# Optimization experiments

Hardware: AMD Instinct MI355X
Metric: run time of the kernel (lower is better)

The kernel has to match this reference:

```python
import jax, jax.numpy as jnp
import numpy as np

# ViT-Small config
L, D, H, HD = 12, 384, 6, 64
P, IMG, NCLS = 16, 224, 1000
NPATCH = (IMG // P) ** 2  # 196
GAMMA, MIN_TOKENS, EPS = 0.5, 16, 1e-6
SCALE = HD ** -0.5


def _ln(x, w, b, eps=1e-6):
    mu = jnp.mean(x, axis=-1, keepdims=True)
    var = jnp.var(x, axis=-1, keepdims=True)
    return (x - mu) * jax.lax.rsqrt(var + eps) * w + b


def _qkv_split(xn, w, b):
    # xn: [B, Nt, D] -> q,k,v each [B, H, Nt, HD]
    B, Nt, _ = xn.shape
    qkv = (xn @ w.T + b).reshape(B, Nt, 3, H, HD).transpose(2, 0, 3, 1, 4)
    return qkv[0], qkv[1], qkv[2]


def _vit_forward(x, patch_w, patch_b, cls_token, pos_embed,
                 ln1_w, ln1_b, qkv_w, qkv_b, proj_w, proj_b,
                 ln2_w, ln2_b, fc1_w, fc1_b, fc2_w, fc2_b,
                 norm_w, norm_b, head_w, head_b, keep_schedule=None):
    B = x.shape[0]
    # patch embed: conv stride 16 -> [B, D, 14, 14] -> [B, 196, D]
    xp = jax.lax.conv_general_dilated(x, patch_w, (P, P), 'VALID',
                                      dimension_numbers=('NCHW', 'OIHW', 'NCHW'))
    xp = xp.reshape(B, D, NPATCH).transpose(0, 2, 1) + patch_b
    cls = jnp.broadcast_to(cls_token, (B, 1, D))
    xt = jnp.concatenate([cls, xp], axis=1) + pos_embed  # [B, 197, D]

    N = NPATCH
    prev_mass = jnp.asarray(1.0, jnp.float32)
    schedule = []
    for l in range(L):
        if keep_schedule is not None:
            keep_idx = keep_schedule[l]
        elif N > MIN_TOKENS:
            # CLS-only attention importance scoring (cheap pass)
            xn = _ln(xt, ln1_w[l], ln1_b[l])
            q, k, v = _qkv_split(xn, qkv_w[l], qkv_b[l])
            a_cls = jax.nn.softmax(jnp.einsum('bhqd,bhkd->bhqk', q[:, :, :1], k) * SCALE, axis=-1)[:, :, 0, :]  # [B,H,Nt]
            vnorm = jnp.linalg.norm(v, axis=-1)  # [B,H,Nt]
            imp = (a_cls * vnorm).mean(axis=1)   # [B,Nt]
            imp_p = imp[:, 1:]                   # patch importance
            mass = jnp.mean(imp_p.sum(-1) / (imp.sum(-1) + EPS))
            keep_ratio = float(jnp.clip(GAMMA * mass / (prev_mass + EPS), 0.0, 1.0))
            N_next = max(MIN_TOKENS, int(N * keep_ratio))
            if N_next < N:
                scores = imp_p.mean(0)  # shared keep set across batch (index_select semantics)
                top = jax.lax.top_k(scores, N_next)[1]
                keep_idx = jnp.concatenate([jnp.zeros((1,), jnp.int32),
                                            jnp.sort(top).astype(jnp.int32) + 1])
            else:
                keep_idx = None
            prev_mass = mass
        else:
            keep_idx = None
        schedule.append(keep_idx)
        if keep_idx is not None:
            xt = jnp.take(xt, keep_idx, axis=1)
            N = int(keep_idx.shape[0]) - 1

        # full transformer block on surviving tokens
        Nt = xt.shape[1]
        xn = _ln(xt, ln1_w[l], ln1_b[l])
        q, k, v = _qkv_split(xn, qkv_w[l], qkv_b[l])
        a = jax.nn.softmax(jnp.einsum('bhqd,bhkd->bhqk', q, k) * SCALE, axis=-1)
        o = jnp.einsum('bhqk,bhkd->bhqd', a, v).transpose(0, 2, 1, 3).reshape(B, Nt, D)
        xt = xt + o @ proj_w[l].T + proj_b[l]
        h = _ln(xt, ln2_w[l], ln2_b[l])
        h = jax.nn.gelu(h @ fc1_w[l].T + fc1_b[l], approximate=False)
        xt = xt + h @ fc2_w[l].T + fc2_b[l]

    xt = _ln(xt, norm_w, norm_b)
    logits = xt[:, 0] @ head_w.T + head_b
    return logits, schedule


def setup_inputs() -> dict:
    key = jax.random.key(0)
    ks = jax.random.split(key, 10)
    rn = lambda k, s, sc=0.02: jax.random.normal(k, s, jnp.float32) * sc
    return {
        'x': jax.random.normal(ks[0], (64, 3, IMG, IMG), jnp.float32),
        'patch_w': rn(ks[1], (D, 3, P, P)),
        'patch_b': jnp.zeros((D,), jnp.float32),
        'cls_token': rn(ks[2], (1, 1, D)),
        'pos_embed': rn(ks[3], (1, NPATCH + 1, D)),
        'ln1_w': jnp.ones((L, D), jnp.float32), 'ln1_b': jnp.zeros((L, D), jnp.float32),
        'qkv_w': rn(ks[4], (L, 3 * D, D)), 'qkv_b': jnp.zeros((L, 3 * D), jnp.float32),
        'proj_w': rn(ks[5], (L, D, D)), 'proj_b': jnp.zeros((L, D), jnp.float32),
        'ln2_w': jnp.ones((L, D), jnp.float32), 'ln2_b': jnp.zeros((L, D), jnp.float32),
        'fc1_w': rn(ks[6], (L, 4 * D, D)), 'fc1_b': jnp.zeros((L, 4 * D), jnp.float32),
        'fc2_w': rn(ks[7], (L, D, 4 * D)), 'fc2_b': jnp.zeros((L, D), jnp.float32),
        'norm_w': jnp.ones((D,), jnp.float32), 'norm_b': jnp.zeros((D,), jnp.float32),
        'head_w': rn(ks[8], (NCLS, D)), 'head_b': jnp.zeros((NCLS,), jnp.float32),
    }


def reference(x, patch_w, patch_b, cls_token, pos_embed, ln1_w, ln1_b, qkv_w, qkv_b,
              proj_w, proj_b, ln2_w, ln2_b, fc1_w, fc1_b, fc2_w, fc2_b,
              norm_w, norm_b, head_w, head_b):
    logits, _ = _vit_forward(x, patch_w, patch_b, cls_token, pos_embed, ln1_w, ln1_b,
                             qkv_w, qkv_b, proj_w, proj_b, ln2_w, ln2_b,
                             fc1_w, fc1_b, fc2_w, fc2_b, norm_w, norm_b, head_w, head_b)
    return logits
```

## Files before the change

### kernel.cpp

```cpp
#include <hip/hip_runtime.h>
#include <hip/hip_bf16.h>

static constexpr int kL = 12;
static constexpr int kD = 384;
static constexpr int kH = 6;
static constexpr int kB = 64;
static constexpr int kNP = 196;
static constexpr int kBAND = 197;
static constexpr int kNCLS = 1000;
static constexpr float kSCALE = 0.125f;
static constexpr float kEPS = 1e-6f;
static constexpr size_t kWQ = (size_t)kB * kH * kBAND * 64;

typedef __attribute__((ext_vector_type(8))) short short8;
typedef __attribute__((ext_vector_type(4))) float f32x4;

__device__ __forceinline__ float gelu_f(float x) {
    return 0.5f * x * (1.0f + erff(x * 0.70710678118654752440f));
}
__device__ __forceinline__ unsigned short f2bf(float x) {
    __hip_bfloat16 h = __float2bfloat16(x);
    return *(unsigned short*)&h;
}

__global__ __launch_bounds__(384) void k_init(int* si, float* sf,
                                              const float* __restrict__ cls,
                                              const float* __restrict__ pos,
                                              float* __restrict__ xtA,
                                              float2* __restrict__ pstats) {
    int b = blockIdx.x, c = threadIdx.x;
    float v = cls[c] + pos[c];
    xtA[(size_t)b * kBAND * kD + c] = v;
    __shared__ float r1[384], r2[384];
    r1[c] = v; r2[c] = v * v;
    __syncthreads();
    if (c < 128) { r1[c] += r1[c + 128] + r1[c + 256]; r2[c] += r2[c + 128] + r2[c + 256]; }
    __syncthreads();
    for (int st = 64; st; st >>= 1) {
        if (c < st) { r1[c] += r1[c + st]; r2[c] += r2[c + st]; }
        __syncthreads();
    }
    if (c == 0) {
        pstats[(size_t)(b * kBAND) * 8 + 0] = make_float2(r1[0], r2[0]);
#pragma unroll
        for (int nn = 1; nn < 6; ++nn) pstats[(size_t)(b * kBAND) * 8 + nn] = make_float2(0.f, 0.f);
        if (b == 0) { si[0] = kBAND; sf[0] = 1.0f; }
    }
}

__global__ __launch_bounds__(256) void k_cvtall(
    const float* __restrict__ s0, const float* __restrict__ s1, const float* __restrict__ s2,
    const float* __restrict__ s3, const float* __restrict__ s4,
    __hip_bfloat16* __restrict__ d0, __hip_bfloat16* __restrict__ d1, __hip_bfloat16* __restrict__ d2,
    __hip_bfloat16* __restrict__ d3, __hip_bfloat16* __restrict__ d4) {
    const int c0 = 73728, c1 = 1400832, c2 = 1843200, c3 = 3612672, c4 = 5382144;
    int stride = gridDim.x * 256;
    for (int i = blockIdx.x * 256 + threadIdx.x; i < c4; i += stride) {
        const float* src; __hip_bfloat16* dst; int off;
        if (i < c0)      { src = s0; dst = d0; off = i; }
        else if (i < c1) { src = s1; dst = d1; off = i - c0; }
        else if (i < c2) { src = s2; dst = d2; off = i - c1; }
        else if (i < c3) { src = s3; dst = d3; off = i - c2; }
        else             { src = s4; dst = d4; off = i - c3; }
        float4 v = ((const float4*)src)[off];
        dst[4 * off + 0] = __float2bfloat16(v.x);
        dst[4 * off + 1] = __float2bfloat16(v.y);
        dst[4 * off + 2] = __float2bfloat16(v.z);
        dst[4 * off + 3] = __float2bfloat16(v.w);
    }
}

__global__ __launch_bounds__(256) void k_im2col(const float* __restrict__ x, __hip_bfloat16* __restrict__ A) {
    int pt = blockIdx.x;
    int b = pt / kNP, t = pt - b * kNP;
    int py = t / 14, px = t - py * 14;
    const float* xb = x + (size_t)b * 3 * 224 * 224;
    __hip_bfloat16* arow = A + (size_t)pt * 768;
    for (int k = threadIdx.x; k < 768; k += 256) {
        int c = k >> 8;
        int r = k & 255;
        int ky = r >> 4, kx = r & 15;
        arow[k] = __float2bfloat16(xb[((size_t)c * 224 + py * 16 + ky) * 224 + px * 16 + kx]);
    }
}

template<int OUT_BF16, int ACT_GELU, int MODE, int LNA, int STATS>
__global__ __launch_bounds__(256) void k_mgemm(
    const void* __restrict__ Av, int lda,
    const unsigned short* __restrict__ W, int K,
    const float* __restrict__ bias,
    void* __restrict__ Cv, int ldc,
    const float* __restrict__ R,
    const int* __restrict__ keepR,
    const float* __restrict__ lnw, const float* __restrict__ lnb,
    int rT, int nT, int band,
    const int* __restrict__ NtPtr, int ntConst,
    const float2* __restrict__ pstatsIn, float2* __restrict__ pstatsOut)
{
    __shared__ __align__(16) unsigned char pool[18432];
    unsigned short (*As)[72] = (unsigned short (*)[72])pool;
    unsigned short (*Ws)[72] = (unsigned short (*)[72])(pool + 9216);
    float (*Cs)[66] = (float (*)[66])pool;
    unsigned short (*Cu)[76] = (unsigned short (*)[76])pool;
    __shared__ float mus[64], rss[64];

    int Nt = NtPtr ? NtPtr[0] : ntConst;
    unsigned int rowsTotal = (unsigned int)kB * (unsigned int)Nt;

    int L = blockIdx.x;
    int xcd = L & 7;
    int m = L >> 3;
    int n = m % nT;
    int r = (m / nT) * 8 + xcd;
    if (r >= rT) return;
    unsigned int r0 = (unsigned int)r * 64;
    int n0 = n * 64;
    if (r0 >= rowsTotal) return;

    int tid = threadIdx.x;
    int srow = tid >> 3;
    int scol = (tid & 7) << 3;

    unsigned int rv0 = r0 + srow, rv1 = r0 + srow + 32;
    bool v0 = rv0 < rowsTotal, v1 = rv1 < rowsTotal;
    const unsigned short* ah0 = nullptr; const unsigned short* ah1 = nullptr;
    const float* af0 = nullptr; const float* af1 = nullptr;
    if (v0) {
        unsigned int bb = rv0 / (unsigned int)Nt, tt = rv0 - bb * Nt;
        size_t prow = (size_t)bb * band + tt;
        if (LNA) af0 = (const float*)Av + prow * lda;
        else     ah0 = (const unsigned short*)Av + prow * lda;
    }
    if (v1) {
        unsigned int bb = rv1 / (unsigned int)Nt, tt = rv1 - bb * Nt;
        size_t prow = (size_t)bb * band + tt;
        if (LNA) af1 = (const float*)Av + prow * lda;
        else     ah1 = (const unsigned short*)Av + prow * lda;
    }
    const unsigned short* wp0 = W + (size_t)(n0 + srow) * K;
    const unsigned short* wp1 = W + (size_t)(n0 + srow + 32) * K;

    float mu0 = 0.f, rs0 = 0.f, mu1 = 0.f, rs1 = 0.f;
    if (LNA) {
        if (tid < 64) {
            unsigned int rv = r0 + tid;
            float mu = 0.f, rsd = 0.f;
            if (rv < rowsTotal) {
                unsigned int bb = rv / (unsigned int)Nt, tt = rv - bb * Nt;
                const float2* ps = pstatsIn + ((size_t)bb * band + tt) * 8;
                float s1 = 0.f, s2 = 0.f;
#pragma unroll
                for (int nn = 0; nn < 6; ++nn) { float2 p = ps[nn]; s1 += p.x; s2 += p.y; }
                mu = s1 * (1.f / 384.f);
                float var = fmaxf(s2 * (1.f / 384.f) - mu * mu, 0.f);
                rsd = rsqrtf(var + kEPS);
            }
            mus[tid] = mu; rss[tid] = rsd;
        }
        __syncthreads();
        mu0 = mus[srow]; rs0 = rss[srow];
        mu1 = mus[srow + 32]; rs1 = rss[srow + 32];
    }

    int wave = tid >> 6, lane = tid & 63;
    int wr32 = ((wave >> 1) & 1) * 32, wc32 = (wave & 1) * 32;
    int l15 = lane & 15, l4 = lane >> 4;

    f32x4 acc00 = {}, acc01 = {}, acc10 = {}, acc11 = {};

    for (int k0 = 0; k0 < K; k0 += 64) {
        uint4 zero = make_uint4(0, 0, 0, 0);
        uint4 a0 = zero, a1 = zero;
        uint4 w0 = *(const uint4*)(wp0 + k0 + scol);
        uint4 w1 = *(const uint4*)(wp1 + k0 + scol);
        if (LNA) {
            float4 lw0 = *(const float4*)(lnw + k0 + scol);
            float4 lw1 = *(const float4*)(lnw + k0 + scol + 4);
            float4 lb0 = *(const float4*)(lnb + k0 + scol);
            float4 lb1 = *(const float4*)(lnb + k0 + scol + 4);
            if (v0) {
                float4 x0 = *(const float4*)(af0 + k0 + scol);
                float4 x1 = *(const float4*)(af0 + k0 + scol + 4);
                unsigned short p[8];
                p[0] = f2bf((x0.x - mu0) * rs0 * lw0.x + lb0.x);
                p[1] = f2bf((x0.y - mu0) * rs0 * lw0.y + lb0.y);
                p[2] = f2bf((x0.z - mu0) * rs0 * lw0.z + lb0.z);
                p[3] = f2bf((x0.w - mu0) * rs0 * lw0.w + lb0.w);
                p[4] = f2bf((x1.x - mu0) * rs0 * lw1.x + lb1.x);
                p[5] = f2bf((x1.y - mu0) * rs0 * lw1.y + lb1.y);
                p[6] = f2bf((x1.z - mu0) * rs0 * lw1.z + lb1.z);
                p[7] = f2bf((x1.w - mu0) * rs0 * lw1.w + lb1.w);
                a0 = *(uint4*)p;
            }
            if (v1) {
                float4 x0 = *(const float4*)(af1 + k0 + scol);
                float4 x1 = *(const float4*)(af1 + k0 + scol + 4);
                unsigned short p[8];
                p[0] = f2bf((x0.x - mu1) * rs1 * lw0.x + lb0.x);
                p[1] = f2bf((x0.y - mu1) * rs1 * lw0.y + lb0.y);
                p[2] = f2bf((x0.z - mu1) * rs1 * lw0.z + lb0.z);
                p[3] = f2bf((x0.w - mu1) * rs1 * lw0.w + lb0.w);
                p[4] = f2bf((x1.x - mu1) * rs1 * lw1.x + lb1.x);
                p[5] = f2bf((x1.y - mu1) * rs1 * lw1.y + lb1.y);
                p[6] = f2bf((x1.z - mu1) * rs1 * lw1.z + lb1.z);
                p[7] = f2bf((x1.w - mu1) * rs1 * lw1.w + lb1.w);
                a1 = *(uint4*)p;
            }
        } else {
            a0 = v0 ? *(const uint4*)(ah0 + k0 + scol) : zero;
            a1 = v1 ? *(const uint4*)(ah1 + k0 + scol) : zero;
        }
        __syncthreads();
        *(uint4*)&As[srow][scol] = a0;
        *(uint4*)&As[srow + 32][scol] = a1;
        *(uint4*)&Ws[srow][scol] = w0;
        *(uint4*)&Ws[srow + 32][scol] = w1;
        __syncthreads();
#pragma unroll
        for (int ks = 0; ks < 2; ++ks) {
            short8 af_0 = *(const short8*)&As[wr32 + l15][ks * 32 + l4 * 8];
            short8 af_1 = *(const short8*)&As[wr32 + 16 + l15][ks * 32 + l4 * 8];
            short8 bf_0 = *(const short8*)&Ws[wc32 + l15][ks * 32 + l4 * 8];
            short8 bf_1 = *(const short8*)&Ws[wc32 + 16 + l15][ks * 32 + l4 * 8];
            acc00 = __builtin_amdgcn_mfma_f32_16x16x32_bf16(af_0, bf_0, acc00, 0, 0, 0);
            acc01 = __builtin_amdgcn_mfma_f32_16x16x32_bf16(af_0, bf_1, acc01, 0, 0, 0);
            acc10 = __builtin_amdgcn_mfma_f32_16x16x32_bf16(af_1, bf_0, acc10, 0, 0, 0);
            acc11 = __builtin_amdgcn_mfma_f32_16x16x32_bf16(af_1, bf_1, acc11, 0, 0, 0);
        }
    }

    __syncthreads();
    f32x4 accs[2][2] = { { acc00, acc01 }, { acc10, acc11 } };
#pragma unroll
    for (int fi = 0; fi < 2; ++fi) {
        int lrow = wr32 + fi * 16 + l4 * 4;
        unsigned int rvb = r0 + lrow;
#pragma unroll
        for (int fj = 0; fj < 2; ++fj) {
            int lcol = wc32 + fj * 16 + l15;
            float bv = bias ? bias[n0 + lcol] : 0.f;
#pragma unroll
            for (int rr = 0; rr < 4; ++rr) {
                unsigned int rv = rvb + rr;
                float v = accs[fi][fj][rr] + bv;
                if (ACT_GELU) v = gelu_f(v);
                if (MODE == 2) {
                    if (rv < rowsTotal) {
                        unsigned int bb = rv / (unsigned int)Nt;
                        unsigned int tt = rv - bb * (unsigned int)Nt;
                        v += R[(size_t)(tt + 1) * kD + n0 + lcol];
                    }
                } else if (R && rv < rowsTotal) {
                    unsigned int bb = rv / (unsigned int)Nt;
                    unsigned int tt = rv - bb * (unsigned int)Nt;
                    size_t rrow = keepR ? ((size_t)bb * band + keepR[tt]) : ((size_t)bb * band + tt);
                    v += R[rrow * ldc + n0 + lcol];
                }
                if (OUT_BF16) Cu[lrow + rr][lcol] = f2bf(v);
                else          Cs[lrow + rr][lcol] = v;
            }
        }
    }
    __syncthreads();

    if (OUT_BF16) {
#pragma unroll
        for (int i = 0; i < 2; ++i) {
            int id = tid + (i << 8);
            int row = id >> 3, c2 = id & 7;
            unsigned int rv = r0 + row;
            if (rv < rowsTotal) {
                unsigned int bb = rv / (unsigned int)Nt;
                unsigned int tt = rv - bb * (unsigned int)Nt;
                size_t prow = (size_t)bb * band + tt;
                uint4 val = *(const uint4*)&Cu[row][c2 << 3];
                *(uint4*)((__hip_bfloat16*)Cv + prow * ldc + n0 + (c2 << 3)) = val;
            }
        }
    } else {
#pragma unroll
        for (int i = 0; i < 4; ++i) {
            int id = tid + (i << 8);
            int row = id >> 4, c4 = id & 15;
            unsigned int rv = r0 + row;
            if (rv < rowsTotal) {
                unsigned int bb = rv / (unsigned int)Nt;
                unsigned int tt = rv - bb * (unsigned int)Nt;
                float4 val = *(const float4*)&Cs[row][c4 << 2];
                if (MODE == 1) {
                    int which = n0 >= 768 ? 2 : (n0 >= 384 ? 1 : 0);
                    int hh = (n0 - which * 384) >> 6;
                    *(float4*)((float*)Cv + (size_t)which * kWQ +
                               (((size_t)bb * kH + hh) * kBAND + tt) * 64 + (c4 << 2)) = val;
                } else if (MODE == 2) {
                    *(float4*)((float*)Cv + ((size_t)bb * kBAND + tt + 1) * ldc + n0 + (c4 << 2)) = val;
                } else {
                    *(float4*)((float*)Cv + ((size_t)bb * band + tt) * ldc + n0 + (c4 << 2)) = val;
                }
                if (STATS) {
                    float s1 = (val.x + val.y) + (val.z + val.w);
                    float s2 = (val.x * val.x + val.y * val.y) + (val.z * val.z + val.w * val.w);
#pragma unroll
                    for (int off = 1; off < 16; off <<= 1) {
                        s1 += __shfl_xor(s1, off, 64);
                        s2 += __shfl_xor(s2, off, 64);
                    }
                    if (c4 == 0) {
                        size_t sridx = (MODE == 2) ? ((size_t)bb * kBAND + tt + 1)
                                                   : ((size_t)bb * band + tt);
                        pstatsOut[sridx * 8 + n] = make_float2(s1, s2);
                    }
                }
            }
        }
    }
}

__global__ __launch_bounds__(256) void k_decA(const float* __restrict__ qsplit,
                                              float* __restrict__ imph, float* __restrict__ sabh,
                                              const int* __restrict__ si) {
    int Nt = si[0];
    if (Nt - 1 <= 16) return;
    int tid = threadIdx.x, w = tid >> 6, lane = tid & 63;
    int bh = blockIdx.x;
    __shared__ float qs[64];
    __shared__ float sdot[224], svn[224];
    __shared__ float red[256];
    const float* qp = qsplit + (size_t)bh * kBAND * 64;
    const float* kp = qsplit + kWQ + (size_t)bh * kBAND * 64;
    const float* vp = qsplit + 2 * kWQ + (size_t)bh * kBAND * 64;
    if (tid < 64) qs[tid] = qp[tid];
    __syncthreads();
    float qv = qs[lane];
    for (int j = w; j < Nt; j += 8) {
        int j2 = j + 4;
        bool has2 = j2 < Nt;
        float k1 = kp[(size_t)j * 64 + lane];
        float v1 = vp[(size_t)j * 64 + lane];
        float k2 = has2 ? kp[(size_t)j2 * 64 + lane] : 0.f;
        float v2 = has2 ? vp[(size_t)j2 * 64 + lane] : 0.f;
        float p1 = qv * k1, n1 = v1 * v1;
        float p2 = qv * k2, n2 = v2 * v2;
#pragma unroll
        for (int off = 1; off < 64; off <<= 1) {
            p1 += __shfl_xor(p1, off, 64); n1 += __shfl_xor(n1, off, 64);
            p2 += __shfl_xor(p2, off, 64); n2 += __shfl_xor(n2, off, 64);
        }
        if (lane == 0) {
            sdot[j] = p1 * kSCALE; svn[j] = sqrtf(n1);
            if (has2) { sdot[j2] = p2 * kSCALE; svn[j2] = sqrtf(n2); }
        }
    }
    __syncthreads();
    float s = (tid < Nt) ? sdot[tid] : -INFINITY;
    red[tid] = s; __syncthreads();
    for (int st = 128; st; st >>= 1) { if (tid < st) red[tid] = fmaxf(red[tid], red[tid + st]); __syncthreads(); }
    float mmax = red[0]; __syncthreads();
    float e = (tid < Nt) ? expf(s - mmax) : 0.f;
    red[tid] = e; __syncthreads();
    for (int st = 128; st; st >>= 1) { if (tid < st) red[tid] += red[tid + st]; __syncthreads(); }
    float inv = 1.f / red[0];
    float val = (tid < Nt) ? e * inv * svn[tid] : 0.f;
    if (tid < Nt) imph[(size_t)bh * kBAND + tid] = val;
    __syncthreads();
    red[tid] = val; __syncthreads();
    for (int st = 128; st; st >>= 1) { if (tid < st) red[tid] += red[tid + st]; __syncthreads(); }
    if (tid == 0) { sabh[2 * bh] = red[0]; sabh[2 * bh + 1] = val; }
}

__global__ __launch_bounds__(256) void k_decB(int* __restrict__ si, float* __restrict__ sf,
                                              const float* __restrict__ imph,
                                              const float* __restrict__ sabh,
                                              int* __restrict__ keep) {
    int Nt = si[0];
    int tid = threadIdx.x;
    if (Nt - 1 <= 16) {
        for (int j = tid; j < Nt; j += 256) keep[j] = j;
        return;
    }
    int N = Nt - 1;
    __shared__ float red[256];
    float v = 0.f;
    if (tid < kB) {
        float sa = 0.f, i0 = 0.f;
#pragma unroll
        for (int hh = 0; hh < kH; ++hh) {
            sa += sabh[2 * (tid * kH + hh)];
            i0 += sabh[2 * (tid * kH + hh) + 1];
        }
        sa *= (1.f / 6.f); i0 *= (1.f / 6.f);
        v = (sa - i0) / (sa + kEPS);
    }
    red[tid] = v; __syncthreads();
    for (int st = 128; st; st >>= 1) { if (tid < st) red[tid] += red[tid + st]; __syncthreads(); }
    float mass = red[0] * (1.f / 64.f);
    float prev = sf[0];
    float ratio = 0.5f * mass / (prev + kEPS);
    ratio = fminf(fmaxf(ratio, 0.f), 1.f);
    int N_next = (int)((double)N * (double)ratio);
    if (N_next < 16) N_next = 16;
    if (tid == 0) sf[0] = mass;
    __syncthreads();
    if (N_next >= N) {
        for (int j = tid; j < Nt; j += 256) keep[j] = j;
        return;
    }
    __shared__ float sc[200];
    __shared__ int flag[200];
    if (tid < N) {
        float a0 = 0.f, a1 = 0.f, a2 = 0.f, a3 = 0.f;
        const float* p = imph + tid + 1;
#pragma unroll 4
        for (int q = 0; q < kB * kH; q += 4) {
            a0 += p[(size_t)(q + 0) * kBAND];
            a1 += p[(size_t)(q + 1) * kBAND];
            a2 += p[(size_t)(q + 2) * kBAND];
            a3 += p[(size_t)(q + 3) * kBAND];
        }
        sc[tid] = (a0 + a1) + (a2 + a3);
    }
    __syncthreads();
    if (tid < N) {
        float s2 = sc[tid];
        int rank = 0;
        for (int i = 0; i < N; ++i) {
            float o2 = sc[i];
            rank += (o2 > s2) || (o2 == s2 && i < tid);
        }
        flag[tid] = (rank < N_next) ? 1 : 0;
    }
    __syncthreads();
    if (tid == 0) {
        keep[0] = 0;
        int pos = 1;
        for (int j = 0; j < N; ++j) if (flag[j]) keep[pos++] = j + 1;
        si[0] = N_next + 1;
    }
}

__global__ __launch_bounds__(256) void k_attn2(const float* __restrict__ qsplit,
                                               __hip_bfloat16* __restrict__ o,
                                               const int* __restrict__ si,
                                               const int* __restrict__ keep) {
    __shared__ __align__(16) unsigned short Kb[224][72];
    __shared__ __align__(16) unsigned short Vt[64][228];
    __shared__ __align__(16) unsigned short Pb[4][16][228];
    int Nt = si[0];
    int bh = blockIdx.x;
    int b = bh / kH, h = bh - b * kH;
    int tid = threadIdx.x, w = tid >> 6, lane = tid & 63;
    int l15 = lane & 15, l4 = lane >> 4;
    int nJT = (Nt + 15) >> 4;
    int nKT = (Nt + 31) >> 5;
    int NTP = nKT << 5;

    const float* qb = qsplit + (size_t)bh * kBAND * 64;
    const float* kb = qsplit + kWQ + (size_t)bh * kBAND * 64;
    const float* vb = qsplit + 2 * kWQ + (size_t)bh * kBAND * 64;

    {
        int rr = tid >> 3;
        int c8 = (tid & 7) << 3;
        for (int r = rr; r < NTP; r += 32) {
            unsigned short ks[8], vs[8];
#pragma unroll
            for (int e = 0; e < 8; ++e) { ks[e] = 0; vs[e] = 0; }
            if (r < Nt) {
                int old = keep[r];
                const float* kr = kb + ((size_t)old << 6) + c8;
                const float* vr = vb + ((size_t)old << 6) + c8;
                float4 k0 = *(const float4*)kr, k1 = *(const float4*)(kr + 4);
                float4 vv0 = *(const float4*)vr, vv1 = *(const float4*)(vr + 4);
                ks[0] = f2bf(k0.x); ks[1] = f2bf(k0.y); ks[2] = f2bf(k0.z); ks[3] = f2bf(k0.w);
                ks[4] = f2bf(k1.x); ks[5] = f2bf(k1.y); ks[6] = f2bf(k1.z); ks[7] = f2bf(k1.w);
                vs[0] = f2bf(vv0.x); vs[1] = f2bf(vv0.y); vs[2] = f2bf(vv0.z); vs[3] = f2bf(vv0.w);
                vs[4] = f2bf(vv1.x); vs[5] = f2bf(vv1.y); vs[6] = f2bf(vv1.z); vs[7] = f2bf(vv1.w);
            }
            *(uint4*)&Kb[r][c8] = *(uint4*)ks;
#pragma unroll
            for (int e = 0; e < 8; ++e) Vt[c8 + e][r] = vs[e];
        }
    }
    __syncthreads();

    for (int strip = w; strip < nJT; strip += 4) {
        int tq = (strip << 4) + l15;
        int told = (tq < Nt) ? keep[tq] : 0;
        const float* qrow = qb + ((size_t)told << 6) + (l4 << 3);
        float4 q0 = *(const float4*)(qrow),      q1 = *(const float4*)(qrow + 4);
        float4 q2 = *(const float4*)(qrow + 32), q3 = *(const float4*)(qrow + 36);
        unsigned short qa[8], qc[8];
        qa[0] = f2bf(q0.x); qa[1] = f2bf(q0.y); qa[2] = f2bf(q0.z); qa[3] = f2bf(q0.w);
        qa[4] = f2bf(q1.x); qa[5] = f2bf(q1.y); qa[6] = f2bf(q1.z); qa[7] = f2bf(q1.w);
        qc[0] = f2bf(q2.x); qc[1] = f2bf(q2.y); qc[2] = f2bf(q2.z); qc[3] = f2bf(q2.w);
        qc[4] = f2bf(q3.x); qc[5] = f2bf(q3.y); qc[6] = f2bf(q3.z); qc[7] = f2bf(q3.w);
        short8 qf0 = *(short8*)qa;
        short8 qf1 = *(short8*)qc;

        f32x4 sv[13];
#pragma unroll
        for (int jt = 0; jt < 13; ++jt) {
            if (jt < nJT) {
                const unsigned short* kr = &Kb[(jt << 4) + l15][l4 << 3];
                short8 kf0 = *(const short8*)(kr);
                short8 kf1 = *(const short8*)(kr + 32);
                f32x4 a = {};
                a = __builtin_amdgcn_mfma_f32_16x16x32_bf16(qf0, kf0, a, 0, 0, 0);
                a = __builtin_amdgcn_mfma_f32_16x16x32_bf16(qf1, kf1, a, 0, 0, 0);
                sv[jt] = a;
            }
        }
        float mx[4] = { -INFINITY, -INFINITY, -INFINITY, -INFINITY };
#pragma unroll
        for (int jt = 0; jt < 13; ++jt) if (jt < nJT) {
            bool ok = ((jt << 4) + l15) < Nt;
#pragma unroll
            for (int r = 0; r < 4; ++r) {
                float s = ok ? sv[jt][r] * kSCALE : -INFINITY;
                sv[jt][r] = s;
                mx[r] = fmaxf(mx[r], s);
            }
        }
#pragma unroll
        for (int r = 0; r < 4; ++r) {
            mx[r] = fmaxf(mx[r], __shfl_xor(mx[r], 1, 64));
            mx[r] = fmaxf(mx[r], __shfl_xor(mx[r], 2, 64));
            mx[r] = fmaxf(mx[r], __shfl_xor(mx[r], 4, 64));
            mx[r] = fmaxf(mx[r], __shfl_xor(mx[r], 8, 64));
        }
        float sm[4] = { 0.f, 0.f, 0.f, 0.f };
#pragma unroll
        for (int jt = 0; jt < 13; ++jt) if (jt < nJT) {
#pragma unroll
            for (int r = 0; r < 4; ++r) {
                float p = expf(sv[jt][r] - mx[r]);
                sv[jt][r] = p;
                sm[r] += p;
            }
        }
#pragma unroll
        for (int r = 0; r < 4; ++r) {
            sm[r] += __shfl_xor(sm[r], 1, 64);
            sm[r] += __shfl_xor(sm[r], 2, 64);
            sm[r] += __shfl_xor(sm[r], 4, 64);
            sm[r] += __shfl_xor(sm[r], 8, 64);
            sm[r] = 1.f / sm[r];
        }
#pragma unroll
        for (int jt = 0; jt < 13; ++jt) if (jt < nJT) {
#pragma unroll
            for (int r = 0; r < 4; ++r)
                Pb[w][(l4 << 2) + r][(jt << 4) + l15] = f2bf(sv[jt][r] * sm[r]);
        }
        for (int c = (nJT << 4) + lane; c < NTP; c += 64) {
#pragma unroll
            for (int rr2 = 0; rr2 < 16; ++rr2) Pb[w][rr2][c] = 0;
        }
        asm volatile("s_waitcnt lgkmcnt(0)" ::: "memory");
        __builtin_amdgcn_sched_barrier(0);

        f32x4 oacc[4] = { {}, {}, {}, {} };
#pragma unroll
        for (int kt = 0; kt < 7; ++kt) if (kt < nKT) {
            short8 pf = *(const short8*)&Pb[w][l15][(kt << 5) + (l4 << 3)];
#pragma unroll
            for (int dt = 0; dt < 4; ++dt) {
                short8 vf = *(const short8*)&Vt[(dt << 4) + l15][(kt << 5) + (l4 << 3)];
                oacc[dt] = __builtin_amdgcn_mfma_f32_16x16x32_bf16(pf, vf, oacc[dt], 0, 0, 0);
            }
        }
#pragma unroll
        for (int dt = 0; dt < 4; ++dt) {
#pragma unroll
            for (int r = 0; r < 4; ++r) {
                int tqo = (strip << 4) + (l4 << 2) + r;
                if (tqo < Nt)
                    o[((size_t)b * kBAND + tqo) * kD + h * 64 + (dt << 4) + l15] =
                        __float2bfloat16(oacc[dt][r]);
            }
        }
    }
}

__global__ __launch_bounds__(256) void k_head(const float* __restrict__ X,
                                              const float* __restrict__ nw, const float* __restrict__ nb,
                                              const float* __restrict__ hw, const float* __restrict__ hb,
                                              float* __restrict__ out) {
    int b = blockIdx.x >> 2;
    int tid = threadIdx.x;
    __shared__ float xs[384];
    __shared__ float red[256];
    const float* row = X + (size_t)b * kBAND * kD;
    float s1 = 0.f, s2 = 0.f;
    for (int c = tid; c < 384; c += 256) { float v = row[c]; xs[c] = v; s1 += v; s2 += v * v; }
    red[tid] = s1; __syncthreads();
    for (int st = 128; st; st >>= 1) { if (tid < st) red[tid] += red[tid + st]; __syncthreads(); }
    float sum = red[0]; __syncthreads();
    red[tid] = s2; __syncthreads();
    for (int st = 128; st; st >>= 1) { if (tid < st) red[tid] += red[tid + st]; __syncthreads(); }
    float sq = red[0];
    float mu = sum * (1.f / 384.f);
    float var = fmaxf(sq * (1.f / 384.f) - mu * mu, 0.f);
    float rs = rsqrtf(var + kEPS);
    __syncthreads();
    for (int c = tid; c < 384; c += 256) xs[c] = (xs[c] - mu) * rs * nw[c] + nb[c];
    __syncthreads();
    int n = ((blockIdx.x & 3) << 8) + tid;
    if (n >= kNCLS) return;
    const float* wrow = hw + (size_t)n * kD;
    float acc = 0.f;
#pragma unroll 8
    for (int d = 0; d < kD; d += 4) {
        float4 w4 = *(const float4*)(wrow + d);
        acc += xs[d] * w4.x + xs[d + 1] * w4.y + xs[d + 2] * w4.z + xs[d + 3] * w4.w;
    }
    out[(size_t)b * kNCLS + n] = acc + hb[n];
}

extern "C" void kernel_launch(void* const* d_in, const int* in_sizes, int n_in,
                              void* d_out, int out_size, void* d_ws, size_t ws_size,
                              hipStream_t stream) {
    const float* x       = (const float*)d_in[0];
    const float* patch_w = (const float*)d_in[1];
    const float* patch_b = (const float*)d_in[2];
    const float* cls_tok = (const float*)d_in[3];
    const float* pos     = (const float*)d_in[4];
    const float* ln1w    = (const float*)d_in[5];
    const float* ln1b    = (const float*)d_in[6];
    const float* qkvw    = (const float*)d_in[7];
    const float* qkvb    = (const float*)d_in[8];
    const float* projw   = (const float*)d_in[9];
    const float* projb   = (const float*)d_in[10];
    const float* ln2w    = (const float*)d_in[11];
    const float* ln2b    = (const float*)d_in[12];
    const float* fc1w    = (const float*)d_in[13];
    const float* fc1b    = (const float*)d_in[14];
    const float* fc2w    = (const float*)d_in[15];
    const float* fc2b    = (const float*)d_in[16];
    const float* normw   = (const float*)d_in[17];
    const float* normb   = (const float*)d_in[18];
    const float* headw   = (const float*)d_in[19];
    const float* headb   = (const float*)d_in[20];
    float* out = (float*)d_out;

    char* ws = (char*)d_ws;
    const size_t MB = 1024ull * 1024ull;
    int*   si   = (int*)ws;
    float* sf   = (float*)(ws + 64);
    int*   keep = (int*)(ws + 256);
    float* sabh = (float*)(ws + 4096);
    float* imph = (float*)(ws + 16384);
    float* xtA  = (float*)(ws + 1 * MB);
    float* xtB  = (float*)(ws + 21 * MB);
    __hip_bfloat16* obuf = (__hip_bfloat16*)(ws + 41 * MB);
    __hip_bfloat16* Aim    = (__hip_bfloat16*)(ws + 51 * MB);
    float*          qsplit = (float*)(ws + 51 * MB);
    __hip_bfloat16* hbuf   = (__hip_bfloat16*)(ws + 51 * MB);
    __hip_bfloat16* wpat = (__hip_bfloat16*)(ws + 110 * MB);
    __hip_bfloat16* wqkv = (__hip_bfloat16*)(ws + 111 * MB);
    __hip_bfloat16* wprj = (__hip_bfloat16*)(ws + 122 * MB);
    __hip_bfloat16* wfc1 = (__hip_bfloat16*)(ws + 126 * MB);
    __hip_bfloat16* wfc2 = (__hip_bfloat16*)(ws + 141 * MB);
    float2* pstats = (float2*)(ws + 156 * MB);

    k_init<<<64, 384, 0, stream>>>(si, sf, cls_tok, pos, xtA, pstats);
    k_cvtall<<<2048, 256, 0, stream>>>(patch_w, qkvw, projw, fc1w, fc2w,
                                       wpat, wqkv, wprj, wfc1, wfc2);

    k_im2col<<<kB * kNP, 256, 0, stream>>>(x, Aim);
    k_mgemm<0, 0, 2, 0, 1><<<8 * 6 * 25, 256, 0, stream>>>(
        (const void*)Aim, 768, (const unsigned short*)wpat, 768,
        patch_b, xtA, kD, pos, (const int*)nullptr,
        (const float*)nullptr, (const float*)nullptr,
        196, 6, 196, (const int*)nullptr, 196,
        (const float2*)nullptr, pstats);

    float* cur = xtA; float* oth = xtB;
    for (int l = 0; l < kL; ++l) {
        const float* l1w = ln1w + l * kD;  const float* l1b = ln1b + l * kD;
        const __hip_bfloat16* qw = wqkv + (size_t)l * 1152 * kD;
        const float* qb = qkvb + l * 1152;
        const __hip_bfloat16* pw = wprj + (size_t)l * kD * kD;
        const float* pb = projb + l * kD;
        const float* l2w = ln2w + l * kD;  const float* l2b = ln2b + l * kD;
        const __hip_bfloat16* f1w = wfc1 + (size_t)l * 1536 * kD;
        const float* f1b = fc1b + l * 1536;
        const __hip_bfloat16* f2w = wfc2 + (size_t)l * kD * 1536;
        const float* f2b = fc2b + l * kD;

        k_mgemm<0, 0, 1, 1, 0><<<8 * 18 * 25, 256, 0, stream>>>(
            (const void*)cur, kD, (const unsigned short*)qw, kD,
            qb, qsplit, 1152, (const float*)nullptr, (const int*)nullptr,
            l1w, l1b, 197, 18, kBAND, si, 0,
            (const float2*)pstats, (float2*)nullptr);
        k_decA<<<kB * kH, 256, 0, stream>>>(qsplit, imph, sabh, si);
        k_decB<<<1, 256, 0, stream>>>(si, sf, imph, sabh, keep);
        k_attn2<<<kB * kH, 256, 0, stream>>>(qsplit, obuf, si, keep);
        k_mgemm<0, 0, 0, 0, 1><<<8 * 6 * 25, 256, 0, stream>>>(
            (const void*)obuf, kD, (const unsigned short*)pw, kD,
            pb, oth, kD, cur, keep,
            (const float*)nullptr, (const float*)nullptr,
            197, 6, kBAND, si, 0,
            (const float2*)nullptr, pstats);
        { float* tmp = cur; cur = oth; oth = tmp; }
        k_mgemm<1, 1, 0, 1, 0><<<8 * 24 * 25, 256, 0, stream>>>(
            (const void*)cur, kD, (const unsigned short*)f1w, kD,
            f1b, hbuf, 1536, (const float*)nullptr, (const int*)nullptr,
            l2w, l2b, 197, 24, kBAND, si, 0,
            (const float2*)pstats, (float2*)nullptr);
        k_mgemm<0, 0, 0, 0, 1><<<8 * 6 * 25, 256, 0, stream>>>(
            (const void*)hbuf, 1536, (const unsigned short*)f2w, 1536,
            f2b, cur, kD, cur, (const int*)nullptr,
            (const float*)nullptr, (const float*)nullptr,
            197, 6, kBAND, si, 0,
            (const float2*)nullptr, pstats);
    }

    k_head<<<kB * 4, 256, 0, stream>>>(cur, normw, normb, headw, headb, out);
}
```

Baseline: 1.262 ms.

## Store QKV split buffer in bf16 instead of fp32

The QKV GEMM now writes its head-split Q/K/V output as bf16, not fp32, so the buffer between kernels is half the size. The scoring kernel and the attention kernel read bf16 directly, and attention loads K, V and Q as packed 16-byte vectors without converting each element. This cuts memory traffic and the conversion work in the attention load path. The trade-off is that the importance scoring now sees bf16-rounded Q, K and V, which could change which tokens are kept when scores are close.

Result: no change. 1.251 ms (-0.9%).

```diff
diff --git a/kernel.cpp b/kernel.cpp
--- a/kernel.cpp
+++ b/kernel.cpp
@@ -21,6 +21,10 @@
 __device__ __forceinline__ unsigned short f2bf(float x) {
     __hip_bfloat16 h = __float2bfloat16(x);
     return *(unsigned short*)&h;
+}
+__device__ __forceinline__ float bf2f(unsigned short u) {
+    __hip_bfloat16 h = *(__hip_bfloat16*)&u;
+    return __bfloat162float(h);
 }
 
 __global__ __launch_bounds__(384) void k_init(int* si, float* sf,
@@ -272,9 +276,16 @@
             if (rv < rowsTotal) {
                 unsigned int bb = rv / (unsigned int)Nt;
                 unsigned int tt = rv - bb * (unsigned int)Nt;
-                size_t prow = (size_t)bb * band + tt;
                 uint4 val = *(const uint4*)&Cu[row][c2 << 3];
-                *(uint4*)((__hip_bfloat16*)Cv + prow * ldc + n0 + (c2 << 3)) = val;
+                if (MODE == 1) {
+                    int which = n0 >= 768 ? 2 : (n0 >= 384 ? 1 : 0);
+                    int hh = (n0 - which * 384) >> 6;
+                    *(uint4*)((__hip_bfloat16*)Cv + (size_t)which * kWQ +
+                              (((size_t)bb * kH + hh) * kBAND + tt) * 64 + (c2 << 3)) = val;
+                } else {
+                    size_t prow = (size_t)bb * band + tt;
+                    *(uint4*)((__hip_bfloat16*)Cv + prow * ldc + n0 + (c2 << 3)) = val;
+                }
             }
         }
     } else {
@@ -287,12 +298,7 @@
                 unsigned int bb = rv / (unsigned int)Nt;
                 unsigned int tt = rv - bb * (unsigned int)Nt;
                 float4 val = *(const float4*)&Cs[row][c4 << 2];
-                if (MODE == 1) {
-                    int which = n0 >= 768 ? 2 : (n0 >= 384 ? 1 : 0);
-                    int hh = (n0 - which * 384) >> 6;
-                    *(float4*)((float*)Cv + (size_t)which * kWQ +
-                               (((size_t)bb * kH + hh) * kBAND + tt) * 64 + (c4 << 2)) = val;
-                } else if (MODE == 2) {
+                if (MODE == 2) {
                     *(float4*)((float*)Cv + ((size_t)bb * kBAND + tt + 1) * ldc + n0 + (c4 << 2)) = val;
                 } else {
                     *(float4*)((float*)Cv + ((size_t)bb * band + tt) * ldc + n0 + (c4 << 2)) = val;
@@ -316,7 +322,7 @@
     }
 }
 
-__global__ __launch_bounds__(256) void k_decA(const float* __restrict__ qsplit,
+__global__ __launch_bounds__(256) void k_decA(const __hip_bfloat16* __restrict__ qsplit,
                                               float* __restrict__ imph, float* __restrict__ sabh,
                                               const int* __restrict__ si) {
     int Nt = si[0];
@@ -326,19 +332,19 @@
     __shared__ float qs[64];
     __shared__ float sdot[224], svn[224];
     __shared__ float red[256];
-    const float* qp = qsplit + (size_t)bh * kBAND * 64;
-    const float* kp = qsplit + kWQ + (size_t)bh * kBAND * 64;
-    const float* vp = qsplit + 2 * kWQ + (size_t)bh * kBAND * 64;
-    if (tid < 64) qs[tid] = qp[tid];
+    const __hip_bfloat16* qp = qsplit + (size_t)bh * kBAND * 64;
+    const __hip_bfloat16* kp = qsplit + kWQ + (size_t)bh * kBAND * 64;
+    const __hip_bfloat16* vp = qsplit + 2 * kWQ + (size_t)bh * kBAND * 64;
+    if (tid < 64) qs[tid] = __bfloat162float(qp[tid]);
     __syncthreads();
     float qv = qs[lane];
     for (int j = w; j < Nt; j += 8) {
         int j2 = j + 4;
         bool has2 = j2 < Nt;
-        float k1 = kp[(size_t)j * 64 + lane];
-        float v1 = vp[(size_t)j * 64 + lane];
-        float k2 = has2 ? kp[(size_t)j2 * 64 + lane] : 0.f;
-        float v2 = has2 ? vp[(size_t)j2 * 64 + lane] : 0.f;
+        float k1 = __bfloat162float(kp[(size_t)j * 64 + lane]);
+        float v1 = __bfloat162float(vp[(size_t)j * 64 + lane]);
+        float k2 = has2 ? __bfloat162float(kp[(size_t)j2 * 64 + lane]) : 0.f;
+        float v2 = has2 ? __bfloat162float(vp[(size_t)j2 * 64 + lane]) : 0.f;
         float p1 = qv * k1, n1 = v1 * v1;
         float p2 = qv * k2, n2 = v2 * v2;
 #pragma unroll
@@ -438,7 +444,7 @@
     }
 }
 
-__global__ __launch_bounds__(256) void k_attn2(const float* __restrict__ qsplit,
+__global__ __launch_bounds__(256) void k_attn2(const __hip_bfloat16* __restrict__ qsplit,
                                                __hip_bfloat16* __restrict__ o,
                                                const int* __restrict__ si,
                                                const int* __restrict__ keep) {
@@ -454,29 +460,22 @@
     int nKT = (Nt + 31) >> 5;
     int NTP = nKT << 5;
 
-    const float* qb = qsplit + (size_t)bh * kBAND * 64;
-    const float* kb = qsplit + kWQ + (size_t)bh * kBAND * 64;
-    const float* vb = qsplit + 2 * kWQ + (size_t)bh * kBAND * 64;
+    const unsigned short* qb = (const unsigned short*)qsplit + (size_t)bh * kBAND * 64;
+    const unsigned short* kb = (const unsigned short*)qsplit + kWQ + (size_t)bh * kBAND * 64;
+    const unsigned short* vb = (const unsigned short*)qsplit + 2 * kWQ + (size_t)bh * kBAND * 64;
 
     {
         int rr = tid >> 3;
         int c8 = (tid & 7) << 3;
         for (int r = rr; r < NTP; r += 32) {
-            unsigned short ks[8], vs[8];
-#pragma unroll
-            for (int e = 0; e < 8; ++e) { ks[e] = 0; vs[e] = 0; }
+            uint4 kv = make_uint4(0, 0, 0, 0), vv = make_uint4(0, 0, 0, 0);
             if (r < Nt) {
                 int old = keep[r];
-                const float* kr = kb + ((size_t)old << 6) + c8;
-                const float* vr = vb + ((size_t)old << 6) + c8;
-                float4 k0 = *(const float4*)kr, k1 = *(const float4*)(kr + 4);
-                float4 vv0 = *(const float4*)vr, vv1 = *(const float4*)(vr + 4);
-                ks[0] = f2bf(k0.x); ks[1] = f2bf(k0.y); ks[2] = f2bf(k0.z); ks[3] = f2bf(k0.w);
-                ks[4] = f2bf(k1.x); ks[5] = f2bf(k1.y); ks[6] = f2bf(k1.z); ks[7] = f2bf(k1.w);
-                vs[0] = f2bf(vv0.x); vs[1] = f2bf(vv0.y); vs[2] = f2bf(vv0.z); vs[3] = f2bf(vv0.w);
-                vs[4] = f2bf(vv1.x); vs[5] = f2bf(vv1.y); vs[6] = f2bf(vv1.z); vs[7] = f2bf(vv1.w);
-            }
-            *(uint4*)&Kb[r][c8] = *(uint4*)ks;
+                kv = *(const uint4*)(kb + ((size_t)old << 6) + c8);
+                vv = *(const uint4*)(vb + ((size_t)old << 6) + c8);
+            }
+            *(uint4*)&Kb[r][c8] = kv;
+            const unsigned short* vs = (const unsigned short*)&vv;
 #pragma unroll
             for (int e = 0; e < 8; ++e) Vt[c8 + e][r] = vs[e];
         }
@@ -486,16 +485,9 @@
     for (int strip = w; strip < nJT; strip += 4) {
         int tq = (strip << 4) + l15;
         int told = (tq < Nt) ? keep[tq] : 0;
-        const float* qrow = qb + ((size_t)told << 6) + (l4 << 3);
-        float4 q0 = *(const float4*)(qrow),      q1 = *(const float4*)(qrow + 4);
-        float4 q2 = *(const float4*)(qrow + 32), q3 = *(const float4*)(qrow + 36);
-        unsigned short qa[8], qc[8];
-        qa[0] = f2bf(q0.x); qa[1] = f2bf(q0.y); qa[2] = f2bf(q0.z); qa[3] = f2bf(q0.w);
-        qa[4] = f2bf(q1.x); qa[5] = f2bf(q1.y); qa[6] = f2bf(q1.z); qa[7] = f2bf(q1.w);
-        qc[0] = f2bf(q2.x); qc[1] = f2bf(q2.y); qc[2] = f2bf(q2.z); qc[3] = f2bf(q2.w);
-        qc[4] = f2bf(q3.x); qc[5] = f2bf(q3.y); qc[6] = f2bf(q3.z); qc[7] = f2bf(q3.w);
-        short8 qf0 = *(short8*)qa;
-        short8 qf1 = *(short8*)qc;
+        const unsigned short* qrow = qb + ((size_t)told << 6) + (l4 << 3);
+        short8 qf0 = *(const short8*)(qrow);
+        short8 qf1 = *(const short8*)(qrow + 32);
 
         f32x4 sv[13];
 #pragma unroll
@@ -654,7 +646,7 @@
     float* xtB  = (float*)(ws + 21 * MB);
     __hip_bfloat16* obuf = (__hip_bfloat16*)(ws + 41 * MB);
     __hip_bfloat16* Aim    = (__hip_bfloat16*)(ws + 51 * MB);
-    float*          qsplit = (float*)(ws + 51 * MB);
+    __hip_bfloat16* qsplit = (__hip_bfloat16*)(ws + 51 * MB);
     __hip_bfloat16* hbuf   = (__hip_bfloat16*)(ws + 51 * MB);
     __hip_bfloat16* wpat = (__hip_bfloat16*)(ws + 110 * MB);
     __hip_bfloat16* wqkv = (__hip_bfloat16*)(ws + 111 * MB);
@@ -688,7 +680,7 @@
         const __hip_bfloat16* f2w = wfc2 + (size_t)l * kD * 1536;
         const float* f2b = fc2b + l * kD;
 
-        k_mgemm<0, 0, 1, 1, 0><<<8 * 18 * 25, 256, 0, stream>>>(
+        k_mgemm<1, 0, 1, 1, 0><<<8 * 18 * 25, 256, 0, stream>>>(
             (const void*)cur, kD, (const unsigned short*)qw, kD,
             qb, qsplit, 1152, (const float*)nullptr, (const int*)nullptr,
             l1w, l1b, 197, 18, kBAND, si, 0,
```
